# Kernel optimization log

Measured on AMD Instinct MI355X. Metric: run time of the kernel, lower is better.

## Reference

```python
import jax, jax.numpy as jnp
import numpy as np

DECAY = 0.8
COMMITMENT = 1.0
EPS = 1e-05


def setup_inputs() -> dict:
    key = jax.random.key(0)
    k1, k2 = jax.random.split(key)
    x = jax.random.normal(k1, (8, 4096, 256), dtype=jnp.float32)
    embed = jax.random.normal(k2, (8192, 256), dtype=jnp.float32)
    cluster_size = jnp.zeros((8192,), dtype=jnp.float32)
    embed_avg = embed  # torch registers embed_avg = embed.clone()
    return {"x": x, "embed": embed, "cluster_size": cluster_size, "embed_avg": embed_avg}


def reference(x, embed, cluster_size, embed_avg):
    # EuclideanCodebook.forward (training mode) + VectorQuantize straight-through.
    K, D = embed.shape
    shape = x.shape
    flatten = x.reshape(-1, D)  # [T, D], T = B*N

    dist = (2.0 * (flatten @ embed.T)
            - jnp.sum(flatten * flatten, axis=-1, keepdims=True)
            - jnp.sum(embed * embed, axis=-1)[None, :])  # [T, K]
    embed_ind = jnp.argmax(dist, axis=-1)  # [T]

    quantize = embed[embed_ind].reshape(shape)  # gather

    # EMA codebook statistics (scatter-add instead of materializing one-hot [T,K])
    bins = jax.ops.segment_sum(jnp.ones_like(embed_ind, dtype=x.dtype), embed_ind, num_segments=K)  # [K]
    embed_sum = jax.ops.segment_sum(flatten, embed_ind, num_segments=K)  # [K, D]

    new_cluster_size = cluster_size * DECAY + (1.0 - DECAY) * bins
    new_embed_avg = embed_avg * DECAY + (1.0 - DECAY) * embed_sum

    total = new_cluster_size.sum()
    smoothed = (new_cluster_size + EPS) / (total + K * EPS) * total  # laplace smoothing
    new_embed = new_embed_avg / smoothed[:, None]

    commit_loss = jnp.mean((jax.lax.stop_gradient(quantize) - x) ** 2) * COMMITMENT
    quantize_st = x + jax.lax.stop_gradient(quantize - x)  # straight-through

    ind_out = embed_ind.reshape(shape[:-1])
    return quantize_st, ind_out, commit_loss, new_embed, new_cluster_size, new_embed_avg
```

## Files before the change

kernel.cpp:

```cpp
#include <hip/hip_runtime.h>

#define DECAYF 0.8f
#define OMDF   0.2f
#define EPSF   1e-5f
#define COMMITF 1.0f
#define MARGINF 0.024f
#define FIXCAP  8192
#define MAXR    64

typedef _Float16 h8v __attribute__((ext_vector_type(8)));
typedef float f4v __attribute__((ext_vector_type(4)));

__device__ inline void gload_lds16(const void* g, void* l) {
  __builtin_amdgcn_global_load_lds(
      (const __attribute__((address_space(1))) unsigned int*)g,
      (__attribute__((address_space(3))) unsigned int*)l, 16, 0, 0);
}

__global__ __launch_bounds__(256) void k_pre(
    const float* __restrict__ embed, char* __restrict__ Ews,
    float* __restrict__ zero_p, int zero_n, float* __restrict__ ee, int K, int D)
{
  const int tid = threadIdx.x;
  const int gid0 = blockIdx.x * 256 + tid;
  const int gstride = gridDim.x * 256;

  for (int i = gid0; i < zero_n; i += gstride) zero_p[i] = 0.0f;

  for (int gid = gid0; gid < K * (D / 8); gid += gstride) {
    int k = gid >> 5;
    int d0 = (gid & 31) * 8;
    const float* ep = embed + (size_t)k * D + d0;
    float4 v0 = *(const float4*)(ep);
    float4 v1 = *(const float4*)(ep + 4);
    float f[8] = {v0.x, v0.y, v0.z, v0.w, v1.x, v1.y, v1.z, v1.w};
    h8v h;
    float ss = 0.f;
#pragma unroll
    for (int e = 0; e < 8; ++e) {
      h[e] = (_Float16)f[e];
      ss = fmaf(f[e], f[e], ss);
    }
    int tt = k >> 6;
    int c = k & 63;
    int byteoff = c * 512 + ((d0 * 2) ^ ((c & 7) << 4));
    *(h8v*)(Ews + (size_t)tt * 32768 + byteoff) = h;
#pragma unroll
    for (int off = 1; off < 32; off <<= 1) ss += __shfl_xor(ss, off);
    if ((gid & 31) == 0) ee[k] = 0.5f * ss;
  }
}

__device__ __forceinline__ void upd2(float s, int code, float& b1, float& b2, int& bi) {
  if (s > b1) { b2 = b1; b1 = s; bi = code; }
  else if (s > b2) { b2 = s; }
}

__device__ __forceinline__ void k_body(
    int TT, int NT, char* lds, const char* Ews, const float* ee,
    int w, int lane, int ch, int l15, int rowbyte0,
    const int (&dbyte)[8],
    const h8v (&xh)[2][8],
    f4v (&CUR)[2][2], f4v (&PRV)[2][2],
    float EEP0, float EEP1, float& EEC0, float& EEC1,
    float (&best)[2][4], float (&bst2)[2][4], int (&bidx)[2][4])
{
  const int k0 = TT * 64;
  const char* cb = lds + (TT & 1) * 32768;
  if (TT + 1 < NT) {
    const char* src = Ews + (size_t)(TT + 1) * 32768 + w * 8192 + lane * 16;
    char* dst = lds + ((TT + 1) & 1) * 32768 + w * 8192;
#pragma unroll
    for (int q = 0; q < 8; ++q) gload_lds16(src + q * 1024, dst + q * 1024);
  }
  EEC0 = ee[k0 + ch * 32 + l15];
  EEC1 = ee[k0 + ch * 32 + l15 + 16];
  const int c0p = k0 - 64 + ch * 32 + l15;
  const int c1p = c0p + 16;
#pragma unroll
  for (int rf = 0; rf < 2; ++rf) {
    CUR[rf][0] = (f4v){0.f, 0.f, 0.f, 0.f};
    CUR[rf][1] = (f4v){0.f, 0.f, 0.f, 0.f};
  }
  h8v Bh0[2], Bh1[2];
  {
    const char* p = cb + rowbyte0 + dbyte[0];
    Bh0[0] = *(const h8v*)(p);
    Bh1[0] = *(const h8v*)(p + 8192);
  }
#pragma unroll
  for (int ks = 0; ks < 8; ++ks) {
    const int cs = ks & 1, ns = cs ^ 1;
    if (ks < 7) {
      const char* p = cb + rowbyte0 + dbyte[ks + 1];
      Bh0[ns] = *(const h8v*)(p);
      Bh1[ns] = *(const h8v*)(p + 8192);
    }
    __builtin_amdgcn_s_setprio(1);
    CUR[0][0] = __builtin_amdgcn_mfma_f32_16x16x32_f16(xh[0][ks], Bh0[cs], CUR[0][0], 0, 0, 0);
    CUR[0][1] = __builtin_amdgcn_mfma_f32_16x16x32_f16(xh[0][ks], Bh1[cs], CUR[0][1], 0, 0, 0);
    CUR[1][0] = __builtin_amdgcn_mfma_f32_16x16x32_f16(xh[1][ks], Bh0[cs], CUR[1][0], 0, 0, 0);
    CUR[1][1] = __builtin_amdgcn_mfma_f32_16x16x32_f16(xh[1][ks], Bh1[cs], CUR[1][1], 0, 0, 0);
    __builtin_amdgcn_s_setprio(0);
    {
      const int rf = ks >> 2, ii = ks & 3;
      upd2(PRV[rf][0][ii] - EEP0, c0p, best[rf][ii], bst2[rf][ii], bidx[rf][ii]);
      upd2(PRV[rf][1][ii] - EEP1, c1p, best[rf][ii], bst2[rf][ii], bidx[rf][ii]);
    }
  }
  __syncthreads();
}

__global__ __launch_bounds__(256, 2) void k_dist(
    const float* __restrict__ x, const char* __restrict__ Ews,
    const float* __restrict__ ee, float* __restrict__ ind_f,
    int* __restrict__ idx_out, int* __restrict__ wl, int* __restrict__ cnt,
    int* __restrict__ cntr, int* __restrict__ rlist,
    int* __restrict__ olist, int* __restrict__ ocnt,
    int T, int K)
{
  extern __shared__ char lds[];
  const int tid = threadIdx.x;
  const int w = tid >> 6, lane = tid & 63;
  const int l15 = lane & 15, lk = lane >> 4;
  const int rgrp = w >> 1, ch = w & 1;
  const int row0 = blockIdx.x * 64 + rgrp * 32;
  const int NT = K / 64;

  h8v xh[2][8];
#pragma unroll
  for (int rf = 0; rf < 2; ++rf) {
    const float* xp = x + (size_t)(row0 + rf * 16 + l15) * 256 + lk * 8;
#pragma unroll
    for (int ks = 0; ks < 8; ++ks) {
      float4 v0 = *(const float4*)(xp + ks * 32);
      float4 v1 = *(const float4*)(xp + ks * 32 + 4);
      float f[8] = {v0.x, v0.y, v0.z, v0.w, v1.x, v1.y, v1.z, v1.w};
      h8v h;
#pragma unroll
      for (int e = 0; e < 8; ++e) h[e] = (_Float16)f[e];
      xh[rf][ks] = h;
    }
  }

  float best[2][4], bst2[2][4];
  int bidx[2][4];
#pragma unroll
  for (int rf = 0; rf < 2; ++rf)
#pragma unroll
    for (int i = 0; i < 4; ++i) { best[rf][i] = -3.0e38f; bst2[rf][i] = -3.0e38f; bidx[rf][i] = 0; }

  const int swz = (l15 & 7) << 4;
  const int rowbyte0 = (ch * 32 + l15) * 512;
  int dbyte[8];
#pragma unroll
  for (int ks = 0; ks < 8; ++ks) dbyte[ks] = (ks * 64 + lk * 16) ^ swz;

  {
    const char* src = Ews + (size_t)w * 8192 + lane * 16;
    char* dst = lds + w * 8192;
#pragma unroll
    for (int q = 0; q < 8; ++q)
      gload_lds16(src + q * 1024, dst + q * 1024);
  }
  __syncthreads();

  f4v accA[2][2], accB[2][2];
#pragma unroll
  for (int rf = 0; rf < 2; ++rf) {
    accB[rf][0] = (f4v){-3.0e38f, -3.0e38f, -3.0e38f, -3.0e38f};
    accB[rf][1] = (f4v){-3.0e38f, -3.0e38f, -3.0e38f, -3.0e38f};
  }
  float eeX0 = 0.f, eeX1 = 0.f, eeY0 = 0.f, eeY1 = 0.f;

  for (int tt = 0; tt < NT; tt += 2) {
    k_body(tt,     NT, lds, Ews, ee, w, lane, ch, l15, rowbyte0, dbyte, xh,
           accA, accB, eeX0, eeX1, eeY0, eeY1, best, bst2, bidx);
    k_body(tt + 1, NT, lds, Ews, ee, w, lane, ch, l15, rowbyte0, dbyte, xh,
           accB, accA, eeY0, eeY1, eeX0, eeX1, best, bst2, bidx);
  }
  {
    const int c0 = (NT - 1) * 64 + ch * 32 + l15, c1 = c0 + 16;
#pragma unroll
    for (int rf = 0; rf < 2; ++rf)
#pragma unroll
      for (int ii = 0; ii < 4; ++ii) {
        upd2(accB[rf][0][ii] - eeX0, c0, best[rf][ii], bst2[rf][ii], bidx[rf][ii]);
        upd2(accB[rf][1][ii] - eeX1, c1, best[rf][ii], bst2[rf][ii], bidx[rf][ii]);
      }
  }

#pragma unroll
  for (int rf = 0; rf < 2; ++rf)
#pragma unroll
    for (int i = 0; i < 4; ++i) {
      float s = best[rf][i], s2 = bst2[rf][i];
      int mi = bidx[rf][i];
#pragma unroll
      for (int off = 1; off < 16; off <<= 1) {
        float os = __shfl_xor(s, off);
        float os2 = __shfl_xor(s2, off);
        int oi = __shfl_xor(mi, off);
        if (os > s || (os == s && oi < mi)) {
          s2 = fmaxf(s, os2);
          s = os; mi = oi;
        } else {
          s2 = fmaxf(s2, os);
        }
      }
      best[rf][i] = s; bst2[rf][i] = s2; bidx[rf][i] = mi;
    }

  float* S  = (float*)lds;
  float* S2 = S + 128;
  int*   MI = (int*)(S2 + 128);
  if (l15 == 0) {
#pragma unroll
    for (int rf = 0; rf < 2; ++rf)
#pragma unroll
      for (int i = 0; i < 4; ++i) {
        int rl = rf * 16 + lk * 4 + i;
        int a = rgrp * 64 + ch * 32 + rl;
        S[a]  = best[rf][i];
        S2[a] = bst2[rf][i];
        MI[a] = bidx[rf][i];
      }
  }
  __syncthreads();
  if (ch == 0 && lane < 32) {
    int a0 = rgrp * 64 + lane;
    float sA = S[a0],      s2A = S2[a0];      int miA = MI[a0];
    float sB = S[a0 + 32], s2B = S2[a0 + 32]; int miB = MI[a0 + 32];
    float s, s2; int mi;
    if (sB > sA || (sB == sA && miB < miA)) { s = sB; mi = miB; s2 = fmaxf(sA, s2B); }
    else                                    { s = sA; mi = miA; s2 = fmaxf(s2A, sB); }
    int row = row0 + lane;
    idx_out[row] = mi;
    ind_f[row] = (float)mi;
    int flagged = 0;
    if (s - s2 < MARGINF) {
      int slot = atomicAdd(cnt, 1);
      if (slot < FIXCAP) { wl[slot] = row; flagged = 1; }
    }
    if (!flagged) {
      int slot2 = atomicAdd(&cntr[mi], 1);
      if (slot2 < MAXR) rlist[mi * MAXR + slot2] = row;
      else { int o = atomicAdd(ocnt, 1); olist[o] = row; }
    }
  }
}

__global__ __launch_bounds__(256) void k_fix1(
    const float* __restrict__ x, const float* __restrict__ embed,
    const float* __restrict__ ee, const int* __restrict__ wl,
    const int* __restrict__ cnt, float* __restrict__ pval,
    int* __restrict__ pidx)
{
  __shared__ float Xs[8][256];
  const int b = blockIdx.x & 255;
  const int g = blockIdx.x >> 8;
  const int t = threadIdx.x;
  int n = *cnt; if (n > FIXCAP) n = FIXCAP;
  const int c = b * 32 + (t & 31);
  const float* er = embed + (size_t)c * 256;
  const float eec = ee[c];
  const int rl = t >> 5;

  for (int r0 = g * 8; r0 < n; r0 += 32) {
    __syncthreads();
    for (int i = t; i < 8 * 64; i += 256) {
      int rr = i >> 6, dq = i & 63;
      int wi = r0 + rr; if (wi >= n) wi = n - 1;
      int row = wl[wi];
      ((float4*)Xs[rr])[dq] = *(const float4*)(x + (size_t)row * 256 + dq * 4);
    }
    __syncthreads();
    const float* xr = Xs[rl];
    float s0 = 0.f, s1 = 0.f, s2a = 0.f, s3 = 0.f;
#pragma unroll
    for (int d = 0; d < 256; d += 16) {
      float4 e0 = *(const float4*)(er + d);
      float4 e1 = *(const float4*)(er + d + 4);
      float4 e2 = *(const float4*)(er + d + 8);
      float4 e3 = *(const float4*)(er + d + 12);
      s0 = fmaf(xr[d + 0], e0.x, s0);  s0 = fmaf(xr[d + 1], e0.y, s0);
      s0 = fmaf(xr[d + 2], e0.z, s0);  s0 = fmaf(xr[d + 3], e0.w, s0);
      s1 = fmaf(xr[d + 4], e1.x, s1);  s1 = fmaf(xr[d + 5], e1.y, s1);
      s1 = fmaf(xr[d + 6], e1.z, s1);  s1 = fmaf(xr[d + 7], e1.w, s1);
      s2a = fmaf(xr[d + 8], e2.x, s2a);  s2a = fmaf(xr[d + 9], e2.y, s2a);
      s2a = fmaf(xr[d + 10], e2.z, s2a); s2a = fmaf(xr[d + 11], e2.w, s2a);
      s3 = fmaf(xr[d + 12], e3.x, s3);  s3 = fmaf(xr[d + 13], e3.y, s3);
      s3 = fmaf(xr[d + 14], e3.z, s3);  s3 = fmaf(xr[d + 15], e3.w, s3);
    }
    float s = ((s0 + s1) + (s2a + s3)) - eec;
    int mi = c;
#pragma unroll
    for (int off = 1; off < 32; off <<= 1) {
      float os = __shfl_xor(s, off);
      int oi = __shfl_xor(mi, off);
      if (os > s || (os == s && oi < mi)) { s = os; mi = oi; }
    }
    int wi = r0 + rl;
    if ((t & 31) == 0 && wi < n) {
      pval[(size_t)wi * 256 + b] = s;
      pidx[(size_t)wi * 256 + b] = mi;
    }
  }
}

__global__ __launch_bounds__(256) void k_fix2(
    const int* __restrict__ wl, const int* __restrict__ cnt,
    const float* __restrict__ pval, const int* __restrict__ pidx,
    float* __restrict__ ind_f, int* __restrict__ idx_out,
    int* __restrict__ cntr, int* __restrict__ rlist,
    int* __restrict__ olist, int* __restrict__ ocnt)
{
  __shared__ float bv[256];
  __shared__ int bi[256];
  const int t = threadIdx.x;
  int n = *cnt; if (n > FIXCAP) n = FIXCAP;
  for (int it = blockIdx.x; it < n; it += gridDim.x) {
    __syncthreads();
    bv[t] = pval[(size_t)it * 256 + t];
    bi[t] = pidx[(size_t)it * 256 + t];
    __syncthreads();
    for (int sh = 128; sh > 0; sh >>= 1) {
      if (t < sh) {
        if (bv[t + sh] > bv[t] || (bv[t + sh] == bv[t] && bi[t + sh] < bi[t])) {
          bv[t] = bv[t + sh]; bi[t] = bi[t + sh];
        }
      }
      __syncthreads();
    }
    if (t == 0) {
      int row = wl[it];
      int kf = bi[0];
      idx_out[row] = kf;
      ind_f[row] = (float)kf;
      int slot = atomicAdd(&cntr[kf], 1);
      if (slot < MAXR) rlist[kf * MAXR + slot] = row;
      else { int o = atomicAdd(ocnt, 1); olist[o] = row; }
    }
  }
}

__global__ __launch_bounds__(256) void k_mid(
    const float* __restrict__ cs, const int* __restrict__ cntr,
    float* __restrict__ ncs, float* __restrict__ total_acc,
    const float* __restrict__ x, const float* __restrict__ embed,
    const int* __restrict__ idx, const int* __restrict__ olist,
    const int* __restrict__ ocnt, float* __restrict__ ovfsum,
    float* __restrict__ quant, float* __restrict__ lslots, int K)
{
  const int tid = threadIdx.x;
  const int wave = tid >> 6, lane = tid & 63;
  int k = blockIdx.x * 256 + tid;
  float v = cs[k] * DECAYF + OMDF * (float)cntr[k];
  ncs[k] = v;
  for (int off = 32; off > 0; off >>= 1) v += __shfl_down(v, off);
  __shared__ float s4[4];
  if ((tid & 63) == 0) s4[tid >> 6] = v;
  __syncthreads();
  if (tid == 0) atomicAdd(total_acc, s4[0] + s4[1] + s4[2] + s4[3]);
  int n = *ocnt;
  for (int i = blockIdx.x * 4 + wave; i < n; i += 128) {
    int row = olist[i];
    int kk = idx[row];
    int d0 = lane * 4;
    float4 xv = *(const float4*)(x + (size_t)row * 256 + d0);
    float4 ev = *(const float4*)(embed + (size_t)kk * 256 + d0);
    atomicAdd(&ovfsum[(size_t)kk * 256 + d0 + 0], xv.x);
    atomicAdd(&ovfsum[(size_t)kk * 256 + d0 + 1], xv.y);
    atomicAdd(&ovfsum[(size_t)kk * 256 + d0 + 2], xv.z);
    atomicAdd(&ovfsum[(size_t)kk * 256 + d0 + 3], xv.w);
    *(float4*)(quant + (size_t)row * 256 + d0) = ev;
    float dx = ev.x - xv.x, dy = ev.y - xv.y, dz = ev.z - xv.z, dw = ev.w - xv.w;
    float l = dx * dx + dy * dy + dz * dz + dw * dw;
    for (int off = 32; off > 0; off >>= 1) l += __shfl_down(l, off);
    if (lane == 0) atomicAdd(&lslots[row & 255], l);
  }
}

__global__ __launch_bounds__(256) void k_ema2(
    const float* __restrict__ x, const float* __restrict__ ea,
    const float* __restrict__ embed,
    const int* __restrict__ cntr, const int* __restrict__ rlist,
    const float* __restrict__ ovfsum, const float* __restrict__ ncs,
    const float* __restrict__ total_acc, float* __restrict__ ne,
    float* __restrict__ nea, float* __restrict__ quant,
    float* __restrict__ lslots, int K, int D)
{
  int wave = threadIdx.x >> 6, lane = threadIdx.x & 63;
  int k = blockIdx.x * 4 + wave;
  if (k >= K) return;
  int c = cntr[k];
  int m = c < MAXR ? c : MAXR;
  int d0 = lane * 4;
  float4 ev = *(const float4*)(embed + (size_t)k * 256 + d0);
  float4 s = *(const float4*)(ovfsum + (size_t)k * 256 + d0);
  float lsum = 0.f;
  for (int i = 0; i < m; ++i) {
    int r = rlist[k * MAXR + i];
    float4 xv = *(const float4*)(x + (size_t)r * 256 + d0);
    s.x += xv.x; s.y += xv.y; s.z += xv.z; s.w += xv.w;
    *(float4*)(quant + (size_t)r * 256 + d0) = ev;
    float dx = ev.x - xv.x, dy = ev.y - xv.y, dz = ev.z - xv.z, dw = ev.w - xv.w;
    lsum += dx * dx + dy * dy + dz * dz + dw * dw;
  }
  float4 eav = *(const float4*)(ea + (size_t)k * 256 + d0);
  float total = *total_acc;
  float csk = ncs[k];
  float sm = (csk + EPSF) / (total + (float)K * EPSF) * total;
  float rs = 1.0f / sm;
  float v0 = eav.x * DECAYF + OMDF * s.x;
  float v1 = eav.y * DECAYF + OMDF * s.y;
  float v2 = eav.z * DECAYF + OMDF * s.z;
  float v3 = eav.w * DECAYF + OMDF * s.w;
  size_t o = (size_t)k * 256 + d0;
  nea[o + 0] = v0; nea[o + 1] = v1; nea[o + 2] = v2; nea[o + 3] = v3;
  ne[o + 0] = v0 * rs; ne[o + 1] = v1 * rs; ne[o + 2] = v2 * rs; ne[o + 3] = v3 * rs;
  for (int off = 32; off > 0; off >>= 1) lsum += __shfl_down(lsum, off);
  if (lane == 0 && m > 0) atomicAdd(&lslots[k & 255], lsum);
}

__global__ void k_loss(const float* __restrict__ lslots, float* __restrict__ out_loss,
                       float scale)
{
  int tid = threadIdx.x;
  float v = lslots[tid];
  for (int off = 32; off > 0; off >>= 1) v += __shfl_down(v, off);
  __shared__ float s4[4];
  if ((tid & 63) == 0) s4[tid >> 6] = v;
  __syncthreads();
  if (tid == 0) out_loss[0] = (s4[0] + s4[1] + s4[2] + s4[3]) * scale;
}

extern "C" void kernel_launch(void* const* d_in, const int* in_sizes, int n_in,
                              void* d_out, int out_size, void* d_ws, size_t ws_size,
                              hipStream_t stream)
{
  const float* x     = (const float*)d_in[0];
  const float* embed = (const float*)d_in[1];
  const float* cs    = (const float*)d_in[2];
  const float* ea    = (const float*)d_in[3];
  const int K = in_sizes[2];
  const int D = in_sizes[1] / K;
  const int T = in_sizes[0] / D;

  float* out   = (float*)d_out;
  float* o_q   = out;
  float* o_ind = out + (size_t)T * D;
  float* o_ls  = o_ind + T;
  float* o_ne  = o_ls + 1;
  float* o_ncs = o_ne + (size_t)K * D;
  float* o_nea = o_ncs + K;

  float* w      = (float*)d_ws;
  float* ee     = w;
  int*   idx    = (int*)(w + K);
  int*   wl     = idx + T;
  float* pval   = (float*)(wl + FIXCAP);
  int*   pidx   = (int*)(pval + (size_t)FIXCAP * 256);
  int*   rlist  = pidx + (size_t)FIXCAP * 256;
  int*   olist  = rlist + (size_t)K * MAXR;
  float* ovfsum = (float*)(olist + T);
  float* lslots = ovfsum + (size_t)K * D;
  float* total  = lslots + 256;
  int*   cnt    = (int*)(total + 1);
  int*   cntr   = cnt + 1;
  int*   ocnt   = cntr + K;
  int zero_n = K * D + 256 + 1 + 1 + K + 1;
  size_t ews_off = (((size_t)(ocnt + 1 - (int*)w)) + 63) & ~(size_t)63;
  char* Ews = (char*)(w + ews_off);

  k_pre<<<2048, 256, 0, stream>>>(embed, Ews, ovfsum, zero_n, ee, K, D);
  k_dist<<<T / 64, 256, 65536, stream>>>(x, Ews, ee, o_ind, idx, wl, cnt,
                                         cntr, rlist, olist, ocnt, T, K);
  k_fix1<<<1024, 256, 0, stream>>>(x, embed, ee, wl, cnt, pval, pidx);
  k_fix2<<<1024, 256, 0, stream>>>(wl, cnt, pval, pidx, o_ind, idx,
                                   cntr, rlist, olist, ocnt);
  k_mid<<<32, 256, 0, stream>>>(cs, cntr, o_ncs, total, x, embed, idx,
                                olist, ocnt, ovfsum, o_q, lslots, K);
  k_ema2<<<(K + 3) / 4, 256, 0, stream>>>(x, ea, embed, cntr, rlist, ovfsum,
                                          o_ncs, total, o_ne, o_nea, o_q, lslots, K, D);
  k_loss<<<1, 256, 0, stream>>>(lslots, o_ls, COMMITF / ((float)T * (float)D));
}
```

Measured before the change: 421.2 us.

## Drop dense overflow-sum buffer and widen LDS swizzle for codebook tiles

Removes the K×D float overflow accumulator, which had to be zeroed every call and read back in the EMA kernel. Overflow rows are now scanned from the overflow list, but only for codes whose count exceeds the per-code row cap. This replaces an 8 MB zeroing pass and a dense read with a rare linear scan, at the risk of a slow scan if overflow is frequent. Separately, the LDS/workspace swizzle for the fp16 codebook gains one more XOR bit, meant to reduce bank conflicts in the distance kernel.

```diff
diff --git a/kernel.cpp b/kernel.cpp
--- a/kernel.cpp
+++ b/kernel.cpp
@@ -43,7 +43,8 @@
     }
     int tt = k >> 6;
     int c = k & 63;
-    int byteoff = c * 512 + ((d0 * 2) ^ ((c & 7) << 4));
+    int swz4 = ((c & 7) << 4) | (((c >> 3) & 1) << 7);
+    int byteoff = c * 512 + ((d0 * 2) ^ swz4);
     *(h8v*)(Ews + (size_t)tt * 32768 + byteoff) = h;
 #pragma unroll
     for (int off = 1; off < 32; off <<= 1) ss += __shfl_xor(ss, off);
@@ -150,7 +151,7 @@
 #pragma unroll
     for (int i = 0; i < 4; ++i) { best[rf][i] = -3.0e38f; bst2[rf][i] = -3.0e38f; bidx[rf][i] = 0; }
 
-  const int swz = (l15 & 7) << 4;
+  const int swz = ((l15 & 7) << 4) | ((l15 >> 3) << 7);
   const int rowbyte0 = (ch * 32 + l15) * 512;
   int dbyte[8];
 #pragma unroll
@@ -349,7 +350,7 @@
     float* __restrict__ ncs, float* __restrict__ total_acc,
     const float* __restrict__ x, const float* __restrict__ embed,
     const int* __restrict__ idx, const int* __restrict__ olist,
-    const int* __restrict__ ocnt, float* __restrict__ ovfsum,
+    const int* __restrict__ ocnt,
     float* __restrict__ quant, float* __restrict__ lslots, int K)
 {
   const int tid = threadIdx.x;
@@ -369,10 +370,6 @@
     int d0 = lane * 4;
     float4 xv = *(const float4*)(x + (size_t)row * 256 + d0);
     float4 ev = *(const float4*)(embed + (size_t)kk * 256 + d0);
-    atomicAdd(&ovfsum[(size_t)kk * 256 + d0 + 0], xv.x);
-    atomicAdd(&ovfsum[(size_t)kk * 256 + d0 + 1], xv.y);
-    atomicAdd(&ovfsum[(size_t)kk * 256 + d0 + 2], xv.z);
-    atomicAdd(&ovfsum[(size_t)kk * 256 + d0 + 3], xv.w);
     *(float4*)(quant + (size_t)row * 256 + d0) = ev;
     float dx = ev.x - xv.x, dy = ev.y - xv.y, dz = ev.z - xv.z, dw = ev.w - xv.w;
     float l = dx * dx + dy * dy + dz * dz + dw * dw;
@@ -385,7 +382,8 @@
     const float* __restrict__ x, const float* __restrict__ ea,
     const float* __restrict__ embed,
     const int* __restrict__ cntr, const int* __restrict__ rlist,
-    const float* __restrict__ ovfsum, const float* __restrict__ ncs,
+    const int* __restrict__ olist, const int* __restrict__ ocnt,
+    const int* __restrict__ idx, const float* __restrict__ ncs,
     const float* __restrict__ total_acc, float* __restrict__ ne,
     float* __restrict__ nea, float* __restrict__ quant,
     float* __restrict__ lslots, int K, int D)
@@ -397,7 +395,7 @@
   int m = c < MAXR ? c : MAXR;
   int d0 = lane * 4;
   float4 ev = *(const float4*)(embed + (size_t)k * 256 + d0);
-  float4 s = *(const float4*)(ovfsum + (size_t)k * 256 + d0);
+  float4 s = (float4){0.f, 0.f, 0.f, 0.f};
   float lsum = 0.f;
   for (int i = 0; i < m; ++i) {
     int r = rlist[k * MAXR + i];
@@ -406,6 +404,16 @@
     *(float4*)(quant + (size_t)r * 256 + d0) = ev;
     float dx = ev.x - xv.x, dy = ev.y - xv.y, dz = ev.z - xv.z, dw = ev.w - xv.w;
     lsum += dx * dx + dy * dy + dz * dz + dw * dw;
+  }
+  if (c > MAXR) {
+    int n = *ocnt;
+    for (int i = 0; i < n; ++i) {
+      int r = olist[i];
+      if (idx[r] == k) {
+        float4 xv = *(const float4*)(x + (size_t)r * 256 + d0);
+        s.x += xv.x; s.y += xv.y; s.z += xv.z; s.w += xv.w;
+      }
+    }
   }
   float4 eav = *(const float4*)(ea + (size_t)k * 256 + d0);
   float total = *total_acc;
@@ -463,25 +471,25 @@
   int*   pidx   = (int*)(pval + (size_t)FIXCAP * 256);
   int*   rlist  = pidx + (size_t)FIXCAP * 256;
   int*   olist  = rlist + (size_t)K * MAXR;
-  float* ovfsum = (float*)(olist + T);
-  float* lslots = ovfsum + (size_t)K * D;
+  float* lslots = (float*)(olist + T);
   float* total  = lslots + 256;
   int*   cnt    = (int*)(total + 1);
   int*   cntr   = cnt + 1;
   int*   ocnt   = cntr + K;
-  int zero_n = K * D + 256 + 1 + 1 + K + 1;
+  int zero_n = 256 + 1 + 1 + K + 1;
   size_t ews_off = (((size_t)(ocnt + 1 - (int*)w)) + 63) & ~(size_t)63;
   char* Ews = (char*)(w + ews_off);
 
-  k_pre<<<2048, 256, 0, stream>>>(embed, Ews, ovfsum, zero_n, ee, K, D);
+  k_pre<<<2048, 256, 0, stream>>>(embed, Ews, lslots, zero_n, ee, K, D);
   k_dist<<<T / 64, 256, 65536, stream>>>(x, Ews, ee, o_ind, idx, wl, cnt,
                                          cntr, rlist, olist, ocnt, T, K);
   k_fix1<<<1024, 256, 0, stream>>>(x, embed, ee, wl, cnt, pval, pidx);
   k_fix2<<<1024, 256, 0, stream>>>(wl, cnt, pval, pidx, o_ind, idx,
                                    cntr, rlist, olist, ocnt);
   k_mid<<<32, 256, 0, stream>>>(cs, cntr, o_ncs, total, x, embed, idx,
-                                olist, ocnt, ovfsum, o_q, lslots, K);
-  k_ema2<<<(K + 3) / 4, 256, 0, stream>>>(x, ea, embed, cntr, rlist, ovfsum,
-                                          o_ncs, total, o_ne, o_nea, o_q, lslots, K, D);
+                                olist, ocnt, o_q, lslots, K);
+  k_ema2<<<(K + 3) / 4, 256, 0, stream>>>(x, ea, embed, cntr, rlist, olist, ocnt,
+                                          idx, o_ncs, total, o_ne, o_nea, o_q,
+                                          lslots, K, D);
   k_loss<<<1, 256, 0, stream>>>(lslots, o_ls, COMMITF / ((float)T * (float)D));
 }
```

New measurement: 1.041 ms. +147.2%, slower.
